# Performance work log

Measured on AMD Instinct MI355X. Metric: run time of the kernel, lower is better.

## Reference

```python
import jax, jax.numpy as jnp
import numpy as np
import math

B, S, H, NH, R = 1, 1024, 4096, 32, 16
HD = H // NH
BLOCK = 64
PRUNE_RATIO = 0.5
NF4_TABLE = jnp.array([
    -1.0, -0.6961928009986877, -0.5250730514526367, -0.39491748809814453,
    -0.28444138169288635, -0.18477343022823334, -0.09105003625154495, 0.0,
    0.07958029955625534, 0.16093020141124725, 0.24611230194568634,
    0.33791524171829224, 0.4407098591327667, 0.5626170039176941,
    0.7229568362236023, 1.0], dtype=jnp.float32)


def dequant_nf4(codes, absmax):
    # codes: [out,in] int4 values in [0,16); absmax: per-64-elem block scale
    vals = NF4_TABLE[codes.reshape(-1)]                 # [out*in]
    vals = vals.reshape(-1, BLOCK) * absmax[:, None]    # blockwise rescale
    return vals.reshape(codes.shape)                    # [out,in]


def setup_inputs() -> dict:
    key = jax.random.key(0)
    ks = jax.random.split(key, 32)
    d = {"x": jax.random.normal(ks[0], (B, S, H), dtype=jnp.float32)}
    i = 1
    for n in ("q", "k", "v", "o"):
        d[f"w_{n}_codes"] = jax.random.randint(ks[i], (H, H), 0, 16, dtype=jnp.int32); i += 1
        d[f"w_{n}_absmax"] = jax.random.uniform(ks[i], (H * H // BLOCK,), dtype=jnp.float32) * 0.06; i += 1
        d[f"b_{n}"] = jax.random.normal(ks[i], (H,), dtype=jnp.float32) * 0.01; i += 1
        d[f"w_{n}_lora_a"] = jax.random.normal(ks[i], (H, R), dtype=jnp.float32) * (1.0 / math.sqrt(H)); i += 1
        d[f"w_{n}_lora_b"] = jax.random.normal(ks[i], (R, H), dtype=jnp.float32) * 0.02; i += 1
    causal = jnp.tril(jnp.ones((S, S), dtype=bool))
    d["attention_mask"] = jnp.where(causal, 0.0, -1e9).astype(jnp.float32)[None, None]
    return d


def _proj(x, codes, absmax, b, la, lb):
    w = dequant_nf4(codes, absmax).T          # [in,out]
    main = x @ w + b
    lora_a = x @ la                            # [B,S,R]
    return main + lora_a @ lb, main, lora_a


def _kth_val(t, use_abs=True):
    flat = jnp.abs(t).ravel() if use_abs else t.ravel()
    k = int(t.size * PRUNE_RATIO)
    return jnp.sort(flat)[k - 1]


def reference(x, w_q_codes, w_q_absmax, b_q, w_q_lora_a, w_q_lora_b,
              w_k_codes, w_k_absmax, b_k, w_k_lora_a, w_k_lora_b,
              w_v_codes, w_v_absmax, b_v, w_v_lora_a, w_v_lora_b,
              w_o_codes, w_o_absmax, b_o, w_o_lora_a, w_o_lora_b,
              attention_mask):
    q, _, _ = _proj(x, w_q_codes, w_q_absmax, b_q, w_q_lora_a, w_q_lora_b)
    k, _, _ = _proj(x, w_k_codes, w_k_absmax, b_k, w_k_lora_a, w_k_lora_b)
    v, _, _ = _proj(x, w_v_codes, w_v_absmax, b_v, w_v_lora_a, w_v_lora_b)
    # [B,S,H] -> [B,NH,S,HD]
    qh = q.reshape(B, S, NH, HD).transpose(0, 2, 1, 3)
    kh = k.reshape(B, S, NH, HD).transpose(0, 2, 1, 3)
    vh = v.reshape(B, S, NH, HD).transpose(0, 2, 1, 3)
    s = jnp.einsum("bhqd,bhkd->bhqk", qh, kh) / math.sqrt(HD) + attention_mask
    a = jax.nn.softmax(s, axis=-1)
    o = jnp.einsum("bhqk,bhkd->bhqd", a, vh)
    o = o.transpose(0, 2, 1, 3).reshape(B, S, H)
    o_final, _, _ = _proj(o, w_o_codes, w_o_absmax, b_o, w_o_lora_a, w_o_lora_b)
    # iteration < 10 branch: magnitude-pruning thresholds via kth smallest value
    kth_vals = jnp.stack([
        _kth_val(x), _kth_val(qh), _kth_val(kh), _kth_val(vh),
        _kth_val(a, use_abs=False), _kth_val(o)])
    return o_final, kth_vals
```

## Files before the change

kernel.cpp:

```cpp
#include <hip/hip_runtime.h>

#define S_LEN  1024
#define H_DIM  4096
#define NHEAD  32
#define HEAD_D 128
#define RANK   16
#define KE3    4160
#define KEO    4128
#define TOTP   ((long)NHEAD * S_LEN * S_LEN)

typedef __bf16 bf16x8 __attribute__((ext_vector_type(8)));
typedef float  f32x4  __attribute__((ext_vector_type(4)));
typedef unsigned short ushort8v __attribute__((ext_vector_type(8)));

#define GLOAD_LDS16(g, l) __builtin_amdgcn_global_load_lds( \
    (const __attribute__((address_space(1))) unsigned int*)(g), \
    (__attribute__((address_space(3))) unsigned int*)(l), 16, 0, 0)

__device__ const float NF4_TAB[16] = {
    -1.0f, -0.6961928009986877f, -0.5250730514526367f, -0.39491748809814453f,
    -0.28444138169288635f, -0.18477343022823334f, -0.09105003625154495f, 0.0f,
    0.07958029955625534f, 0.16093020141124725f, 0.24611230194568634f,
    0.33791524171829224f, 0.4407098591327667f, 0.5626170039176941f,
    0.7229568362236023f, 1.0f};

__device__ __forceinline__ unsigned short f2bf(float f) {
    unsigned int u = __builtin_bit_cast(unsigned int, f);
    u = (u + 0x7FFFu + ((u >> 16) & 1u)) >> 16;
    return (unsigned short)u;
}

__device__ __forceinline__ float bf2f(unsigned short s) {
    return __builtin_bit_cast(float, (unsigned int)s << 16);
}

__device__ __forceinline__ void dequant_body(
    const int* __restrict__ codes, const float* __restrict__ absmax,
    unsigned short* __restrict__ out, long i, int ostride) {
    int4 c0 = *(const int4*)(codes + i);
    int4 c1 = *(const int4*)(codes + i + 4);
    float am = absmax[i >> 6];
    long orow = i >> 12;
    int  col  = (int)(i & 4095);
    ushort8v r;
    r[0] = f2bf(NF4_TAB[c0.x] * am);
    r[1] = f2bf(NF4_TAB[c0.y] * am);
    r[2] = f2bf(NF4_TAB[c0.z] * am);
    r[3] = f2bf(NF4_TAB[c0.w] * am);
    r[4] = f2bf(NF4_TAB[c1.x] * am);
    r[5] = f2bf(NF4_TAB[c1.y] * am);
    r[6] = f2bf(NF4_TAB[c1.z] * am);
    r[7] = f2bf(NF4_TAB[c1.w] * am);
    *(ushort8v*)(out + orow * ostride + col) = r;
}

__global__ __launch_bounds__(256) void prep_weights(
    const int* __restrict__ c0, const int* __restrict__ c1,
    const int* __restrict__ c2, const int* __restrict__ c3,
    const float* __restrict__ a0, const float* __restrict__ a1,
    const float* __restrict__ a2, const float* __restrict__ a3,
    const float* __restrict__ lb0, const float* __restrict__ lb1,
    const float* __restrict__ lb2, const float* __restrict__ lb3,
    const float* __restrict__ b0, const float* __restrict__ b1,
    const float* __restrict__ b2,
    const float* __restrict__ x, const float* __restrict__ la0,
    const float* __restrict__ la1, const float* __restrict__ la2,
    unsigned short* __restrict__ wqkv, unsigned short* __restrict__ wo,
    float* __restrict__ bias3, unsigned short* __restrict__ xb_ext,
    unsigned int* __restrict__ hist, long n) {
    __shared__ float xs[4096];
    int p = blockIdx.y;
    long bx = blockIdx.x;
    int tid = threadIdx.x;
    if (bx < 8192) {
        const int* codes = (p == 0) ? c0 : (p == 1) ? c1 : (p == 2) ? c2 : c3;
        const float* am  = (p == 0) ? a0 : (p == 1) ? a1 : (p == 2) ? a2 : a3;
        long i = (bx * 256 + tid) * 8;
        if (i >= n) return;
        if (p < 3) dequant_body(codes, am, wqkv + (size_t)p * H_DIM * KE3, i, KE3);
        else       dequant_body(codes, am, wo, i, KEO);
        return;
    }
    if (bx < 9216) {
        if (p < 3) {
            long g = (bx - 8192) * 256 + tid;
            int row = (int)(g >> 6), c = (int)(g & 63);
            const float* lb = (p == 0) ? lb0 : (p == 1) ? lb1 : lb2;
            unsigned int r = (unsigned int)(c - 16 * p);
            float v = (r < 16u) ? lb[r * H_DIM + row] : 0.f;
            wqkv[(size_t)p * H_DIM * KE3 + (long)row * KE3 + 4096 + c] = f2bf(v);
            if (g < H_DIM) {
                const float* bp = (p == 0) ? b0 : (p == 1) ? b1 : b2;
                bias3[(size_t)p * H_DIM + g] = bp[g];
            }
            return;
        }
        if (bx < 8704) {
            long g = (bx - 8192) * 256 + tid;
            if (g >= (long)H_DIM * 32) return;
            int row = (int)(g >> 5), c = (int)(g & 31);
            float v = (c < 16) ? lb3[c * H_DIM + row] : 0.f;
            wo[(long)row * KEO + 4096 + c] = f2bf(v);
            return;
        }
        if (bx < 9088) {
            long g = (bx - 8704) * 256 + tid;
            if (g < 6 * 16384) hist[g] = 0u;
        }
        return;
    }
    if (p != 0) return;
    int m = (int)(bx - 9216);
    const float* xr = x + (long)m * H_DIM;
    int c = tid * 16;
    float4 f0 = *(const float4*)(xr + c);
    float4 f1 = *(const float4*)(xr + c + 4);
    float4 f2 = *(const float4*)(xr + c + 8);
    float4 f3 = *(const float4*)(xr + c + 12);
    *(float4*)(xs + c)      = f0;
    *(float4*)(xs + c + 4)  = f1;
    *(float4*)(xs + c + 8)  = f2;
    *(float4*)(xs + c + 12) = f3;
    ushort8v r0, r1;
    r0[0] = f2bf(f0.x); r0[1] = f2bf(f0.y); r0[2] = f2bf(f0.z); r0[3] = f2bf(f0.w);
    r0[4] = f2bf(f1.x); r0[5] = f2bf(f1.y); r0[6] = f2bf(f1.z); r0[7] = f2bf(f1.w);
    r1[0] = f2bf(f2.x); r1[1] = f2bf(f2.y); r1[2] = f2bf(f2.z); r1[3] = f2bf(f2.w);
    r1[4] = f2bf(f3.x); r1[5] = f2bf(f3.y); r1[6] = f2bf(f3.z); r1[7] = f2bf(f3.w);
    unsigned short* orow = xb_ext + (long)m * KE3 + c;
    *(ushort8v*)orow = r0;
    *(ushort8v*)(orow + 8) = r1;
    __syncthreads();
    int w = tid >> 6, lane = tid & 63;
    if (w < 3) {
        const float* la = (w == 0) ? la0 : (w == 1) ? la1 : la2;
        float s[16];
#pragma unroll
        for (int r = 0; r < 16; ++r) s[r] = 0.f;
        for (int k = lane; k < H_DIM; k += 64) {
            float xv = xs[k];
            const float4* lr = (const float4*)(la + (long)k * RANK);
            float4 q0 = lr[0], q1 = lr[1], q2 = lr[2], q3 = lr[3];
            s[0] += xv * q0.x;  s[1] += xv * q0.y;  s[2] += xv * q0.z;  s[3] += xv * q0.w;
            s[4] += xv * q1.x;  s[5] += xv * q1.y;  s[6] += xv * q1.z;  s[7] += xv * q1.w;
            s[8] += xv * q2.x;  s[9] += xv * q2.y;  s[10] += xv * q2.z; s[11] += xv * q2.w;
            s[12] += xv * q3.x; s[13] += xv * q3.y; s[14] += xv * q3.z; s[15] += xv * q3.w;
        }
        for (int off = 32; off; off >>= 1)
#pragma unroll
            for (int r = 0; r < 16; ++r) s[r] += __shfl_xor(s[r], off);
        if (lane == 0)
#pragma unroll
            for (int r = 0; r < 16; ++r)
                xb_ext[(long)m * KE3 + 4096 + 16 * w + r] = f2bf(s[r]);
    } else if (lane < 16) {
        xb_ext[(long)m * KE3 + 4144 + lane] = 0;
    }
}

__global__ __launch_bounds__(256) void lora_ao_kernel(
    unsigned short* __restrict__ ob_ext, const float* __restrict__ la) {
    int m = blockIdx.x;
    const unsigned short* xr = ob_ext + (long)m * KEO;
    int tid = threadIdx.x, lane = tid & 63, wid = tid >> 6;
    float s[4] = {0.f, 0.f, 0.f, 0.f};
    for (int k = lane; k < H_DIM; k += 64) {
        float xv = bf2f(xr[k]);
        const float* lr = la + (long)k * RANK + wid * 4;
        s[0] += xv * lr[0]; s[1] += xv * lr[1];
        s[2] += xv * lr[2]; s[3] += xv * lr[3];
    }
    for (int off = 32; off; off >>= 1)
        for (int r = 0; r < 4; ++r) s[r] += __shfl_down(s[r], off);
    if (lane == 0)
        for (int r = 0; r < 4; ++r) {
            ob_ext[(long)m * KEO + 4096 + wid * 4 + r] = f2bf(s[r]);
            ob_ext[(long)m * KEO + 4112 + wid * 4 + r] = 0;
        }
}

__global__ __launch_bounds__(256) void gemm_nt(
    const unsigned short* __restrict__ A, const unsigned short* __restrict__ B,
    void* __restrict__ Cv, void* __restrict__ Cv2, const float* __restrict__ bias,
    int K, int lda, int ldb, int ldc,
    long strideA, long strideB, long strideC, float alpha, int mode, int obf,
    const unsigned short* __restrict__ tsrc, unsigned short* __restrict__ tdst) {
    __shared__ unsigned short As[128][32];
    __shared__ unsigned short Bs[128][32];
    const int tid = threadIdx.x;
    int bm, bn;
    int k0s = 0, k0e = K;
    if (mode == 1) {
        int i = blockIdx.x;
        if (i >= 36) {
            unsigned short (*tl)[33] = (unsigned short(*)[33])&As[0][0];
            int tb = (i - 36) + 4 * blockIdx.z;
            int tx = tid & 31, ty = tid >> 5;
            for (int tile = tb; tile < 4096; tile += 128) {
                int tc = tile & 127, ts = tile >> 7;
                int c0 = tc * 32, s0 = ts * 32;
                for (int j = 0; j < 32; j += 8)
                    tl[ty + j][tx] = tsrc[(long)(s0 + ty + j) * H_DIM + c0 + tx];
                __syncthreads();
                for (int j = 0; j < 32; j += 8)
                    tdst[(long)(c0 + ty + j) * S_LEN + s0 + tx] = tl[tx][ty + j];
                __syncthreads();
            }
            return;
        }
        int tm = (int)((sqrtf(8.f * i + 1.f) - 1.f) * 0.5f);
        if ((tm + 1) * (tm + 2) / 2 <= i) tm++;
        if (tm * (tm + 1) / 2 > i) tm--;
        int tn = i - tm * (tm + 1) / 2;
        bm = tm * 128; bn = tn * 128;
    } else {
        bm = blockIdx.y * 128; bn = blockIdx.x * 128;
        if (mode == 2) { int kl = bm + 128; if (kl < k0e) k0e = kl; }
    }
    const unsigned short* Ab = A;
    const unsigned short* Bb = B;
    long coff = 0;
    void* Cuse = Cv;
    if (mode == 3) {
        int Kh = (K / 2) & ~31;
        k0s = blockIdx.z ? Kh : 0;
        k0e = blockIdx.z ? K : Kh;
        Cuse = blockIdx.z ? Cv2 : Cv;
    } else {
        Ab += (long)blockIdx.z * strideA;
        Bb += (long)blockIdx.z * strideB;
        coff = (long)blockIdx.z * strideC;
    }
    const int lane = tid & 63, wid = tid >> 6;
    const int wm = (wid >> 1) * 64, wn = (wid & 1) * 64;
    const int sr = wid * 16 + (lane >> 2);
    const int sc = (lane & 3) * 8;
    const unsigned short* gA0 = Ab + (long)(bm + sr) * lda + sc;
    const unsigned short* gA1 = gA0 + (long)64 * lda;
    const unsigned short* gB0 = Bb + (long)(bn + sr) * ldb + sc;
    const unsigned short* gB1 = gB0 + (long)64 * ldb;
    unsigned short* lA0 = &As[wid * 16][0];
    unsigned short* lA1 = &As[64 + wid * 16][0];
    unsigned short* lB0 = &Bs[wid * 16][0];
    unsigned short* lB1 = &Bs[64 + wid * 16][0];
    f32x4 acc[4][4] = {};
    const int kq = (lane >> 4) * 8;
    const int rr = lane & 15;
    for (int k0 = k0s; k0 < k0e; k0 += 32) {
        GLOAD_LDS16(gA0 + k0, lA0);
        GLOAD_LDS16(gA1 + k0, lA1);
        GLOAD_LDS16(gB0 + k0, lB0);
        GLOAD_LDS16(gB1 + k0, lB1);
        __syncthreads();
        bf16x8 af[4], bfr[4];
        for (int i = 0; i < 4; ++i) {
            uint4 ta = *(const uint4*)&As[wm + i * 16 + rr][kq];
            uint4 tb = *(const uint4*)&Bs[wn + i * 16 + rr][kq];
            af[i]  = __builtin_bit_cast(bf16x8, ta);
            bfr[i] = __builtin_bit_cast(bf16x8, tb);
        }
        for (int i = 0; i < 4; ++i)
            for (int j = 0; j < 4; ++j)
                acc[i][j] = __builtin_amdgcn_mfma_f32_16x16x32_bf16(
                    af[i], bfr[j], acc[i][j], 0, 0, 0);
        __syncthreads();
    }
    const int cr = (lane >> 4) * 4;
    const int cc = lane & 15;
    float bv[4];
#pragma unroll
    for (int j = 0; j < 4; ++j)
        bv[j] = bias ? bias[(long)blockIdx.z * H_DIM + bn + wn + j * 16 + cc] : 0.f;
    if (obf) {
        unsigned short* Cb = (unsigned short*)Cuse + coff;
        for (int i = 0; i < 4; ++i)
            for (int j = 0; j < 4; ++j) {
                unsigned short* cp = Cb + (long)(bm + wm + i * 16 + cr) * ldc
                                        + (bn + wn + j * 16 + cc);
                for (int r = 0; r < 4; ++r)
                    cp[(long)r * ldc] = f2bf(acc[i][j][r] * alpha + bv[j]);
            }
    } else {
        float* Cb = (float*)Cuse + coff;
        for (int i = 0; i < 4; ++i)
            for (int j = 0; j < 4; ++j) {
                float* cp = Cb + (long)(bm + wm + i * 16 + cr) * ldc
                               + (bn + wn + j * 16 + cc);
                for (int r = 0; r < 4; ++r)
                    cp[(long)r * ldc] = acc[i][j][r] * alpha + bv[j];
            }
    }
}

__global__ __launch_bounds__(256) void softmax_causal(unsigned short* __restrict__ scores16) {
    int b = blockIdx.x;
    int h = b >> 9, pr = b & 511;
    int tid = threadIdx.x, lane = tid & 63, wid = tid >> 6;
    __shared__ float red[4], red2[4];
    for (int half = 0; half < 2; ++half) {
        int i = half ? (S_LEN - 1 - pr) : pr;
        unsigned short* row = scores16 + ((long)h * S_LEN + i) * S_LEN;
        int L = i + 1;
        float v[4];
        float mx = -1e30f;
        for (int t = 0; t < 4; ++t) {
            int j = tid + (t << 8);
            v[t] = (j < L) ? bf2f(row[j]) : -1e30f;
            mx = fmaxf(mx, v[t]);
        }
        for (int off = 32; off; off >>= 1) mx = fmaxf(mx, __shfl_xor(mx, off));
        if (lane == 0) red[wid] = mx;
        __syncthreads();
        mx = fmaxf(fmaxf(red[0], red[1]), fmaxf(red[2], red[3]));
        float e[4], sum = 0.f;
        for (int t = 0; t < 4; ++t) {
            int j = tid + (t << 8);
            e[t] = (j < L) ? __expf(v[t] - mx) : 0.f;
            sum += e[t];
        }
        for (int off = 32; off; off >>= 1) sum += __shfl_xor(sum, off);
        if (lane == 0) red2[wid] = sum;
        __syncthreads();
        sum = red2[0] + red2[1] + red2[2] + red2[3];
        float inv = 1.f / sum;
        for (int t = 0; t < 4; ++t) {
            int j = tid + (t << 8);
            row[j] = f2bf(e[t] * inv);
        }
        __syncthreads();
    }
}

__global__ __launch_bounds__(256, 2) void hist6(
    const float* __restrict__ x, const unsigned short* __restrict__ qkv,
    const unsigned short* __restrict__ ob, const unsigned short* __restrict__ P,
    unsigned int* __restrict__ hist) {
    __shared__ unsigned int lh[16384];
    const long SH = (long)S_LEN * H_DIM;
    int t = threadIdx.x;
    int b = blockIdx.x;
    int ten, b0, nblk;
    if (b < 256)      { ten = 0; b0 = 0;   nblk = 256; }
    else if (b < 384) { ten = 1; b0 = 256; nblk = 128; }
    else if (b < 512) { ten = 2; b0 = 384; nblk = 128; }
    else if (b < 640) { ten = 3; b0 = 512; nblk = 128; }
    else if (b < 768) { ten = 4; b0 = 640; nblk = 128; }
    else              { ten = 5; b0 = 768; nblk = 768; }
    unsigned int* gh = hist + (long)ten * 16384;
    for (int k = t; k < 16384; k += 256) lh[k] = 0u;
    __syncthreads();
    long i = (long)(b - b0) * 256 + t;
    long stride = (long)nblk * 256;
    if (ten == 0) {
        for (; i < SH / 4; i += stride) {
            float4 v = *(const float4*)(x + i * 4);
            unsigned int u0 = (__builtin_bit_cast(unsigned int, v.x) & 0x7FFFFFFFu) >> 16;
            unsigned int u1 = (__builtin_bit_cast(unsigned int, v.y) & 0x7FFFFFFFu) >> 16;
            unsigned int u2 = (__builtin_bit_cast(unsigned int, v.z) & 0x7FFFFFFFu) >> 16;
            unsigned int u3 = (__builtin_bit_cast(unsigned int, v.w) & 0x7FFFFFFFu) >> 16;
            atomicAdd(&lh[u0 < 16384u ? u0 : 16383u], 1u);
            atomicAdd(&lh[u1 < 16384u ? u1 : 16383u], 1u);
            atomicAdd(&lh[u2 < 16384u ? u2 : 16383u], 1u);
            atomicAdd(&lh[u3 < 16384u ? u3 : 16383u], 1u);
        }
    } else if (ten <= 3) {
        const unsigned short* src = qkv + (size_t)(ten - 1) * SH;
        for (; i < SH / 8; i += stride) {
            ushort8v v = ((const ushort8v*)src)[i];
#pragma unroll
            for (int j = 0; j < 8; ++j) {
                unsigned int u = v[j] & 0x7FFFu;
                atomicAdd(&lh[u < 16384u ? u : 16383u], 1u);
            }
        }
    } else if (ten == 4) {
        for (; i < SH / 8; i += stride) {
            long off = (i >> 9) * KEO + ((i & 511) << 3);
            ushort8v v = *(const ushort8v*)(ob + off);
#pragma unroll
            for (int j = 0; j < 8; ++j) {
                unsigned int u = v[j] & 0x7FFFu;
                atomicAdd(&lh[u < 16384u ? u : 16383u], 1u);
            }
        }
    } else {
        unsigned int zc = 0;
        for (; i < TOTP / 8; i += stride) {
            ushort8v v = ((const ushort8v*)P)[i];
#pragma unroll
            for (int j = 0; j < 8; ++j) {
                unsigned int bb = v[j];
                if (bb == 0) zc++;
                else atomicAdd(&lh[bb < 16384u ? bb : 16383u], 1u);
            }
        }
        if (zc) atomicAdd(&lh[0], zc);
    }
    __syncthreads();
    for (int k = t; k < 16384; k += 256) {
        unsigned int c = lh[k];
        if (c) atomicAdd(&gh[k], c);
    }
}

__global__ __launch_bounds__(256) void finish_kernel(
    float* __restrict__ out, const float* __restrict__ part,
    const float* __restrict__ bias, const unsigned int* __restrict__ hist,
    float* __restrict__ out_kth) {
    int b = blockIdx.x;
    int t = threadIdx.x;
    if (b < 4096) {
        long idx = ((long)b * 256 + t) * 4;
        int n = (int)(idx & 4095);
        float4 o = *(float4*)(out + idx);
        float4 p = *(const float4*)(part + idx);
        float4 bb = *(const float4*)(bias + n);
        o.x += p.x + bb.x; o.y += p.y + bb.y; o.z += p.z + bb.z; o.w += p.w + bb.w;
        *(float4*)(out + idx) = o;
        return;
    }
    int ten = b - 4096;
    const unsigned int* h = hist + (long)ten * 16384;
    __shared__ unsigned int partl[256];
    unsigned int s = 0;
    for (int bb = 0; bb < 64; ++bb) s += h[t * 64 + bb];
    partl[t] = s;
    __syncthreads();
    if (t == 0) {
        long k = (ten == 5) ? TOTP / 2 : (long)S_LEN * H_DIM / 2;
        long c = 0;
        int ch = 0;
        for (; ch < 256; ++ch) {
            if (c + (long)partl[ch] >= k) break;
            c += partl[ch];
        }
        int bin = ch * 64;
        for (;; ++bin) {
            unsigned int hv = h[bin];
            if (c + (long)hv >= k) break;
            c += hv;
        }
        int slot = (ten == 4) ? 5 : (ten == 5) ? 4 : ten;
        out_kth[slot] = __builtin_bit_cast(float, (unsigned int)bin << 16);
    }
}

extern "C" void kernel_launch(void* const* d_in, const int* in_sizes, int n_in,
                              void* d_out, int out_size, void* d_ws, size_t ws_size,
                              hipStream_t stream) {
    (void)in_sizes; (void)n_in; (void)out_size; (void)ws_size;
    const float* x = (const float*)d_in[0];
    const int*   wcodes[4] = {(const int*)d_in[1], (const int*)d_in[6],
                              (const int*)d_in[11], (const int*)d_in[16]};
    const float* wabs[4]   = {(const float*)d_in[2], (const float*)d_in[7],
                              (const float*)d_in[12], (const float*)d_in[17]};
    const float* bias[4]   = {(const float*)d_in[3], (const float*)d_in[8],
                              (const float*)d_in[13], (const float*)d_in[18]};
    const float* lA[4]     = {(const float*)d_in[4], (const float*)d_in[9],
                              (const float*)d_in[14], (const float*)d_in[19]};
    const float* lB[4]     = {(const float*)d_in[5], (const float*)d_in[10],
                              (const float*)d_in[15], (const float*)d_in[20]};

    char* wp = (char*)d_ws;
    auto alloc = [&](size_t bytes) {
        char* p = wp; wp += (bytes + 255) & ~(size_t)255; return p;
    };
    const size_t SH  = (size_t)S_LEN * H_DIM;
    const long   nW  = (long)H_DIM * H_DIM;
    unsigned short* xb_ext = (unsigned short*)alloc((size_t)S_LEN * KE3 * 2);
    unsigned short* qkvb   = (unsigned short*)alloc(3 * SH * 2);
    unsigned short* vT     = (unsigned short*)alloc(SH * 2);
    unsigned short* ob_ext = (unsigned short*)alloc((size_t)S_LEN * KEO * 2);
    unsigned short* Wd_ext = (unsigned short*)alloc((size_t)H_DIM * KEO * 2);
    float*        opart  = (float*)alloc(SH * 4);
    float*        bias3  = (float*)alloc(3 * H_DIM * 4);
    unsigned int* hist   = (unsigned int*)alloc(6 * 16384 * 4);
    char* bigbuf = alloc((size_t)3 * H_DIM * KE3 * 2);
    unsigned short* Wqkv_ext = (unsigned short*)bigbuf;
    unsigned short* scores16 = (unsigned short*)bigbuf;

    float* out_final = (float*)d_out;
    float* out_kth   = out_final + SH;

    unsigned short* qb = qkvb;
    unsigned short* kb = qkvb + SH;
    unsigned short* vb = qkvb + 2 * SH;

    prep_weights<<<dim3(10240, 4), 256, 0, stream>>>(
        wcodes[0], wcodes[1], wcodes[2], wcodes[3],
        wabs[0], wabs[1], wabs[2], wabs[3],
        lB[0], lB[1], lB[2], lB[3],
        bias[0], bias[1], bias[2],
        x, lA[0], lA[1], lA[2],
        Wqkv_ext, Wd_ext, bias3, xb_ext, hist, nW);

    gemm_nt<<<dim3(32, 8, 3), 256, 0, stream>>>(
        xb_ext, Wqkv_ext, qkvb, nullptr, bias3, KE3, KE3, KE3, H_DIM,
        0, (long)H_DIM * KE3, (long)SH, 1.0f, 0, 1, nullptr, nullptr);

    gemm_nt<<<dim3(40, 1, NHEAD), 256, 0, stream>>>(
        qb, kb, scores16, nullptr, nullptr, HEAD_D, H_DIM, H_DIM, S_LEN,
        128, 128, (long)S_LEN * S_LEN, 0.08838834764831845f, 1, 1, vb, vT);

    softmax_causal<<<NHEAD * S_LEN / 2, 256, 0, stream>>>(scores16);

    gemm_nt<<<dim3(1, 8, NHEAD), 256, 0, stream>>>(
        scores16, vT, ob_ext, nullptr, nullptr, S_LEN,
        S_LEN, S_LEN, KEO,
        (long)S_LEN * S_LEN, (long)HEAD_D * S_LEN, 128, 1.0f, 2, 1, nullptr, nullptr);

    lora_ao_kernel<<<S_LEN, 256, 0, stream>>>(ob_ext, lA[3]);

    gemm_nt<<<dim3(32, 8, 2), 256, 0, stream>>>(
        ob_ext, Wd_ext, out_final, opart, nullptr, KEO, KEO, KEO, H_DIM,
        0, 0, 0, 1.0f, 3, 0, nullptr, nullptr);

    hist6<<<1536, 256, 0, stream>>>(x, qkvb, ob_ext, scores16, hist);

    finish_kernel<<<4102, 256, 0, stream>>>(out_final, opart, bias[3], hist, out_kth);
}
```

Before: 776.7 us.

## Double GEMM K-tile to 64 with XOR-swizzled LDS and templated mode

Raises the GEMM K step from 32 to 64 per LDS stage, halving the number of barrier-synchronized iterations, and applies an XOR swizzle to the LDS layout to avoid bank conflicts on the wider rows. The kernel mode becomes a template parameter so per-mode branches resolve at compile time, and loops are fully unrolled. The output-projection K padding grows to 4160 so it is a multiple of 64, which requires adjusting prep_weights, the LoRA-A zero fill, and the split-K boundary. This doubles LDS use per block and adds a little padding work.

```diff
diff --git a/kernel.cpp b/kernel.cpp
--- a/kernel.cpp
+++ b/kernel.cpp
@@ -6,7 +6,7 @@
 #define HEAD_D 128
 #define RANK   16
 #define KE3    4160
-#define KEO    4128
+#define KEO    4160
 #define TOTP   ((long)NHEAD * S_LEN * S_LEN)
 
 typedef __bf16 bf16x8 __attribute__((ext_vector_type(8)));
@@ -82,9 +82,9 @@
         return;
     }
     if (bx < 9216) {
+        long g = (bx - 8192) * 256 + tid;
+        int row = (int)(g >> 6), c = (int)(g & 63);
         if (p < 3) {
-            long g = (bx - 8192) * 256 + tid;
-            int row = (int)(g >> 6), c = (int)(g & 63);
             const float* lb = (p == 0) ? lb0 : (p == 1) ? lb1 : lb2;
             unsigned int r = (unsigned int)(c - 16 * p);
             float v = (r < 16u) ? lb[r * H_DIM + row] : 0.f;
@@ -95,16 +95,13 @@
             }
             return;
         }
-        if (bx < 8704) {
-            long g = (bx - 8192) * 256 + tid;
-            if (g >= (long)H_DIM * 32) return;
-            int row = (int)(g >> 5), c = (int)(g & 31);
-            float v = (c < 16) ? lb3[c * H_DIM + row] : 0.f;
-            wo[(long)row * KEO + 4096 + c] = f2bf(v);
-            return;
-        }
-        if (bx < 9088) {
-            long g = (bx - 8704) * 256 + tid;
+        float v = (c < 16) ? lb3[c * H_DIM + row] : 0.f;
+        wo[(long)row * KEO + 4096 + c] = f2bf(v);
+        return;
+    }
+    if (p == 1) {
+        if (bx < 9600) {
+            long g = (bx - 9216) * 256 + tid;
             if (g < 6 * 16384) hist[g] = 0u;
         }
         return;
@@ -171,25 +168,27 @@
     }
     for (int off = 32; off; off >>= 1)
         for (int r = 0; r < 4; ++r) s[r] += __shfl_down(s[r], off);
-    if (lane == 0)
-        for (int r = 0; r < 4; ++r) {
+    if (lane == 0) {
+        for (int r = 0; r < 4; ++r)
             ob_ext[(long)m * KEO + 4096 + wid * 4 + r] = f2bf(s[r]);
-            ob_ext[(long)m * KEO + 4112 + wid * 4 + r] = 0;
-        }
-}
-
+        for (int r = 0; r < 12; ++r)
+            ob_ext[(long)m * KEO + 4112 + wid * 12 + r] = 0;
+    }
+}
+
+template<int MODE>
 __global__ __launch_bounds__(256) void gemm_nt(
     const unsigned short* __restrict__ A, const unsigned short* __restrict__ B,
     void* __restrict__ Cv, void* __restrict__ Cv2, const float* __restrict__ bias,
     int K, int lda, int ldb, int ldc,
-    long strideA, long strideB, long strideC, float alpha, int mode, int obf,
+    long strideA, long strideB, long strideC, float alpha,
     const unsigned short* __restrict__ tsrc, unsigned short* __restrict__ tdst) {
-    __shared__ unsigned short As[128][32];
-    __shared__ unsigned short Bs[128][32];
+    __shared__ unsigned short As[128][64];
+    __shared__ unsigned short Bs[128][64];
     const int tid = threadIdx.x;
     int bm, bn;
     int k0s = 0, k0e = K;
-    if (mode == 1) {
+    if (MODE == 1) {
         int i = blockIdx.x;
         if (i >= 36) {
             unsigned short (*tl)[33] = (unsigned short(*)[33])&As[0][0];
@@ -214,14 +213,14 @@
         bm = tm * 128; bn = tn * 128;
     } else {
         bm = blockIdx.y * 128; bn = blockIdx.x * 128;
-        if (mode == 2) { int kl = bm + 128; if (kl < k0e) k0e = kl; }
+        if (MODE == 2) { int kl = bm + 128; if (kl < k0e) k0e = kl; }
     }
     const unsigned short* Ab = A;
     const unsigned short* Bb = B;
     long coff = 0;
     void* Cuse = Cv;
-    if (mode == 3) {
-        int Kh = (K / 2) & ~31;
+    if (MODE == 3) {
+        int Kh = (K / 2) & ~63;
         k0s = blockIdx.z ? Kh : 0;
         k0e = blockIdx.z ? K : Kh;
         Cuse = blockIdx.z ? Cv2 : Cv;
@@ -232,33 +231,42 @@
     }
     const int lane = tid & 63, wid = tid >> 6;
     const int wm = (wid >> 1) * 64, wn = (wid & 1) * 64;
-    const int sr = wid * 16 + (lane >> 2);
-    const int sc = (lane & 3) * 8;
-    const unsigned short* gA0 = Ab + (long)(bm + sr) * lda + sc;
-    const unsigned short* gA1 = gA0 + (long)64 * lda;
-    const unsigned short* gB0 = Bb + (long)(bn + sr) * ldb + sc;
-    const unsigned short* gB1 = gB0 + (long)64 * ldb;
-    unsigned short* lA0 = &As[wid * 16][0];
-    unsigned short* lA1 = &As[64 + wid * 16][0];
-    unsigned short* lB0 = &Bs[wid * 16][0];
-    unsigned short* lB1 = &Bs[64 + wid * 16][0];
+    const int srow = lane >> 3;
+    const int scol = ((lane & 7) ^ srow) << 3;
+    const int r0 = wid * 8 + srow;
+    const unsigned short* gA0 = Ab + (long)(bm + r0) * lda + scol;
+    const unsigned short* gB0 = Bb + (long)(bn + r0) * ldb + scol;
     f32x4 acc[4][4] = {};
-    const int kq = (lane >> 4) * 8;
-    const int rr = lane & 15;
-    for (int k0 = k0s; k0 < k0e; k0 += 32) {
-        GLOAD_LDS16(gA0 + k0, lA0);
-        GLOAD_LDS16(gA1 + k0, lA1);
-        GLOAD_LDS16(gB0 + k0, lB0);
-        GLOAD_LDS16(gB1 + k0, lB1);
+    const int q = lane >> 4, rr = lane & 15;
+    const int colh0 = ((q ^ (rr & 7)) << 3);
+    const int colh1 = colh0 ^ 32;
+    for (int k0 = k0s; k0 < k0e; k0 += 64) {
+#pragma unroll
+        for (int p = 0; p < 4; ++p) {
+            GLOAD_LDS16(gA0 + (long)p * 32 * lda + k0, &As[p * 32 + wid * 8][0]);
+            GLOAD_LDS16(gB0 + (long)p * 32 * ldb + k0, &Bs[p * 32 + wid * 8][0]);
+        }
         __syncthreads();
         bf16x8 af[4], bfr[4];
+#pragma unroll
         for (int i = 0; i < 4; ++i) {
-            uint4 ta = *(const uint4*)&As[wm + i * 16 + rr][kq];
-            uint4 tb = *(const uint4*)&Bs[wn + i * 16 + rr][kq];
-            af[i]  = __builtin_bit_cast(bf16x8, ta);
-            bfr[i] = __builtin_bit_cast(bf16x8, tb);
-        }
+            af[i]  = __builtin_bit_cast(bf16x8, *(const uint4*)&As[wm + i * 16 + rr][colh0]);
+            bfr[i] = __builtin_bit_cast(bf16x8, *(const uint4*)&Bs[wn + i * 16 + rr][colh0]);
+        }
+#pragma unroll
         for (int i = 0; i < 4; ++i)
+#pragma unroll
+            for (int j = 0; j < 4; ++j)
+                acc[i][j] = __builtin_amdgcn_mfma_f32_16x16x32_bf16(
+                    af[i], bfr[j], acc[i][j], 0, 0, 0);
+#pragma unroll
+        for (int i = 0; i < 4; ++i) {
+            af[i]  = __builtin_bit_cast(bf16x8, *(const uint4*)&As[wm + i * 16 + rr][colh1]);
+            bfr[i] = __builtin_bit_cast(bf16x8, *(const uint4*)&Bs[wn + i * 16 + rr][colh1]);
+        }
+#pragma unroll
+        for (int i = 0; i < 4; ++i)
+#pragma unroll
             for (int j = 0; j < 4; ++j)
                 acc[i][j] = __builtin_amdgcn_mfma_f32_16x16x32_bf16(
                     af[i], bfr[j], acc[i][j], 0, 0, 0);
@@ -270,7 +278,7 @@
 #pragma unroll
     for (int j = 0; j < 4; ++j)
         bv[j] = bias ? bias[(long)blockIdx.z * H_DIM + bn + wn + j * 16 + cc] : 0.f;
-    if (obf) {
+    if (MODE != 3) {
         unsigned short* Cb = (unsigned short*)Cuse + coff;
         for (int i = 0; i < 4; ++i)
             for (int j = 0; j < 4; ++j) {
@@ -493,26 +501,26 @@
         x, lA[0], lA[1], lA[2],
         Wqkv_ext, Wd_ext, bias3, xb_ext, hist, nW);
 
-    gemm_nt<<<dim3(32, 8, 3), 256, 0, stream>>>(
+    gemm_nt<0><<<dim3(32, 8, 3), 256, 0, stream>>>(
         xb_ext, Wqkv_ext, qkvb, nullptr, bias3, KE3, KE3, KE3, H_DIM,
-        0, (long)H_DIM * KE3, (long)SH, 1.0f, 0, 1, nullptr, nullptr);
-
-    gemm_nt<<<dim3(40, 1, NHEAD), 256, 0, stream>>>(
+        0, (long)H_DIM * KE3, (long)SH, 1.0f, nullptr, nullptr);
+
+    gemm_nt<1><<<dim3(40, 1, NHEAD), 256, 0, stream>>>(
         qb, kb, scores16, nullptr, nullptr, HEAD_D, H_DIM, H_DIM, S_LEN,
-        128, 128, (long)S_LEN * S_LEN, 0.08838834764831845f, 1, 1, vb, vT);
+        128, 128, (long)S_LEN * S_LEN, 0.08838834764831845f, vb, vT);
 
     softmax_causal<<<NHEAD * S_LEN / 2, 256, 0, stream>>>(scores16);
 
-    gemm_nt<<<dim3(1, 8, NHEAD), 256, 0, stream>>>(
+    gemm_nt<2><<<dim3(1, 8, NHEAD), 256, 0, stream>>>(
         scores16, vT, ob_ext, nullptr, nullptr, S_LEN,
         S_LEN, S_LEN, KEO,
-        (long)S_LEN * S_LEN, (long)HEAD_D * S_LEN, 128, 1.0f, 2, 1, nullptr, nullptr);
+        (long)S_LEN * S_LEN, (long)HEAD_D * S_LEN, 128, 1.0f, nullptr, nullptr);
 
     lora_ao_kernel<<<S_LEN, 256, 0, stream>>>(ob_ext, lA[3]);
 
-    gemm_nt<<<dim3(32, 8, 2), 256, 0, stream>>>(
+    gemm_nt<3><<<dim3(32, 8, 2), 256, 0, stream>>>(
         ob_ext, Wd_ext, out_final, opart, nullptr, KEO, KEO, KEO, H_DIM,
-        0, 0, 0, 1.0f, 3, 0, nullptr, nullptr);
+        0, 0, 0, 1.0f, nullptr, nullptr);
 
     hist6<<<1536, 256, 0, stream>>>(x, qkvb, ob_ext, scores16, hist);
 
```

Result: faster. 720.8 us (-7.2%).
